# Kernel optimization log

Measured on AMD Instinct MI355X. Metric: run time of the kernel, lower is better.

Reference implementation:

```python
import jax, jax.numpy as jnp
import numpy as np

B, N, C = 4, 4096, 16
HID, OUT = 64, 64
ALL_K, K = 128, 32          # k + k_pos = 32
KD, KDP = 8, 6              # k_dilated, k_dilated_pos
EPS = 1e-5
NEG_SLOPE = 0.2


def setup_inputs() -> dict:
    ks = jax.random.split(jax.random.key(0), 12)
    C2, C4 = 2 * C, 4 * C
    return {
        "x": jax.random.normal(ks[0], (B, N, C), jnp.float32),
        "pos": jax.random.normal(ks[1], (B, N, 3), jnp.float32),
        "W1": jax.random.normal(ks[2], (C2, C2), jnp.float32) * 0.1,
        "g1": jnp.ones((C2,), jnp.float32),
        "b1": jnp.zeros((C2,), jnp.float32),
        "W2": jax.random.normal(ks[3], (HID, C4), jnp.float32) * 0.05,
        "g2": jnp.ones((HID,), jnp.float32),
        "b2": jnp.zeros((HID,), jnp.float32),
        "W3": jax.random.normal(ks[4], (OUT, HID), jnp.float32) * 0.05,
        "g3": jnp.ones((OUT,), jnp.float32),
        "b3": jnp.zeros((OUT,), jnp.float32),
    }


def pdist2(a):
    # squared pairwise distances (same top-k ordering as cdist p=2, and
    # avoids sqrt(0) on the diagonal). a: (B,N,D) -> (B,N,N)
    sq = jnp.sum(a * a, axis=-1)
    d = sq[:, :, None] + sq[:, None, :] - 2.0 * jnp.einsum('bnd,bmd->bnm', a, a)
    return jnp.maximum(d, 0.0)


def knn_excl_self(d2, k):
    # k nearest excluding self (self is the unique 0-distance nearest point)
    idx = jax.lax.top_k(-d2, k + 1)[1]
    return idx[..., 1:]


def fps(pts, npoint):
    # pts: (M, Kn, 3). Deterministic start at index 0 (torch version uses a
    # random start; only the sampled index set differs, math is identical).
    M, Kn, _ = pts.shape
    rows = jnp.arange(M)

    def body(i, state):
        centroids, distance, farthest = state
        centroids = centroids.at[:, i].set(farthest)
        centroid = pts[rows, farthest][:, None, :]            # (M,1,3)
        dist = jnp.sum((pts - centroid) ** 2, axis=-1)         # (M,Kn)
        distance = jnp.minimum(distance, dist)
        farthest = jnp.argmax(distance, axis=-1).astype(jnp.int32)
        return centroids, distance, farthest

    init = (jnp.zeros((M, npoint), jnp.int32),
            jnp.full((M, Kn), 1e10, jnp.float32),
            jnp.zeros((M,), jnp.int32))
    centroids, _, _ = jax.lax.fori_loop(0, npoint, body, init)
    return centroids


def edge_feat(feat, idx):
    # feat: (B,N,D) node features, idx: (B,N,Kn) neighbor indices
    # returns cat(neighbor - center, center): (B,N,Kn,2D)  (edge_function 249)
    nbr = feat[jnp.arange(feat.shape[0])[:, None, None], idx]  # (B,N,Kn,D)
    ctr = feat[:, :, None, :]
    return jnp.concatenate([nbr - ctr, jnp.broadcast_to(ctr, nbr.shape)], axis=-1)


def bn_lrelu(h, g, b):
    # BatchNorm2d with track_running_stats=False -> always batch stats.
    # h: (B,N,Kn,Cc), stats over (B,N,Kn) per channel.
    mu = jnp.mean(h, axis=(0, 1, 2), keepdims=True)
    var = jnp.var(h, axis=(0, 1, 2), keepdims=True)
    h = (h - mu) * jax.lax.rsqrt(var + EPS) * g + b
    return jnp.where(h > 0, h, NEG_SLOPE * h)


def reference(x, pos, W1, g1, b1, W2, g2, b2, W3, g3, b3):
    # --- dilated neighborhood: all_k nearest by position, FPS down to k ---
    cd2 = pdist2(pos)                                   # (B,N,N)
    idx_l = jax.lax.top_k(-cd2, ALL_K)[1]               # (B,N,ALL_K) incl. self
    idx_l_flat = idx_l.reshape(B * N, ALL_K)
    pts = pos.reshape(B * N, 3)[idx_l_flat]             # (B*N, ALL_K, 3)
    idx_fps_local = fps(pts, K)                         # (B*N, K)
    idx_fps = jnp.take_along_axis(idx_l_flat, idx_fps_local, axis=1)
    idx_fps = idx_fps.reshape(B, N, K)                  # (B,N,K)

    # --- dual kNN graph: k_dilated by feature distance + k_dilated_pos by pos ---
    idx_feat = knn_excl_self(pdist2(x), KD)             # (B,N,KD)
    idx_pos = knn_excl_self(cd2, KDP)                   # (B,N,KDP)
    idx1 = jnp.concatenate([idx_feat, idx_pos], axis=2)  # (B,N,KD+KDP)

    # --- conv1x1-BN-LeakyReLU on dual-graph edge features, max over nbrs ---
    e1 = edge_feat(x, idx1)                             # (B,N,14,2C)
    h1 = bn_lrelu(jnp.einsum('bnkc,oc->bnko', e1, W1), g1, b1)
    f1 = jnp.max(h1, axis=2)                            # (B,N,2C)

    # --- edge features on FPS-dilated graph, two conv1x1-BN-LeakyReLU ---
    e2 = edge_feat(f1, idx_fps)                         # (B,N,K,4C)
    h2 = bn_lrelu(jnp.einsum('bnkc,hc->bnkh', e2, W2), g2, b2)
    h3 = bn_lrelu(jnp.einsum('bnkh,oh->bnko', h2, W3), g3, b3)
    out = jnp.max(h3, axis=2)                           # (B,N,OUT)
    return out, idx1
```

## Files before the change

### kernel.cpp

```cpp
#include <hip/hip_runtime.h>

#define NPTS 4096
#define BNROWS 16384

__device__ __forceinline__ float lrelu(float h) { return h > 0.f ? h : 0.2f * h; }

#define WSYNC asm volatile("s_waitcnt lgkmcnt(0)" ::: "memory")

__device__ __forceinline__ float rfl(float v) {
  return __int_as_float(__builtin_amdgcn_readfirstlane(__float_as_int(v)));
}

__global__ __launch_bounds__(256) void norms_kernel(
    const float* __restrict__ x, float* __restrict__ sqx)
{
  int r = blockIdx.x * 256 + threadIdx.x;
  const float4* xp = (const float4*)(x + (size_t)r * 16);
  float4 a0 = xp[0], a1 = xp[1], a2 = xp[2], a3 = xp[3];
  float s = a0.x*a0.x + a0.y*a0.y + a0.z*a0.z + a0.w*a0.w
          + a1.x*a1.x + a1.y*a1.y + a1.z*a1.z + a1.w*a1.w
          + a2.x*a2.x + a2.y*a2.y + a2.z*a2.z + a2.w*a2.w
          + a3.x*a3.x + a3.y*a3.y + a3.z*a3.z + a3.w*a3.w;
  sqx[r] = s;
}

__global__ __launch_bounds__(512) void knn_pos_kernel(
    const float* __restrict__ pos, int* __restrict__ idx_l,
    int* __restrict__ idx1_i, float* __restrict__ idx1_f)
{
  __shared__ unsigned long long cKey[8][512];
  __shared__ unsigned int cCnt[8];
  int tid = threadIdx.x;
  int w = tid >> 6, lane = tid & 63;
  int r = blockIdx.x * 8 + w;
  int b = r >> 12, n = r & 4095;
  const float* pb = pos + (size_t)b * NPTS * 3;
  float cx = pb[n*3+0], cy = pb[n*3+1], cz = pb[n*3+2];
  if (lane == 0) cCnt[w] = 0u;
  WSYNC;

  unsigned int qp[32];
  int m1 = 65536, m2 = 65536, m3 = 65536;
  #pragma unroll
  for (int t = 0; t < 32; ++t) {
    unsigned int wq = 0u;
    #pragma unroll
    for (int h = 0; h < 2; ++h) {
      int j = (2*t + h) * 64 + lane;
      float dx = cx - pb[j*3+0], dy = cy - pb[j*3+1], dz = cz - pb[j*3+2];
      float d2 = dx*dx + dy*dy + dz*dz;
      int q = (int)(d2 * 1000.0f);
      q = q < 0 ? 0 : (q > 65535 ? 65535 : q);
      wq |= ((unsigned int)q) << (16*h);
      int nm1 = min(m1, q);
      int nm2 = min(m2, max(m1, q));
      int nm3 = min(m3, max(m2, q));
      m1 = nm1; m2 = nm2; m3 = nm3;
    }
    qp[t] = wq;
  }
  int lo = 0, hi = 65535;
  #pragma unroll
  for (int it = 0; it < 16; ++it) {
    int mid = (lo + hi) >> 1;
    int cnt = __popcll(__ballot(m3 <= mid));
    if (cnt >= 43) hi = mid; else lo = mid + 1;
  }
  unsigned int qt = (unsigned int)lo + 2u;

  #pragma unroll
  for (int t = 0; t < 32; ++t) {
    unsigned int wq = qp[t];
    unsigned int q0 = wq & 0xffffu, q1 = wq >> 16;
    if (q0 <= qt) { unsigned int p = atomicAdd(&cCnt[w], 1u); if (p < 512u) cKey[w][p] = (unsigned long long)((2*t)*64 + lane); }
    if (q1 <= qt) { unsigned int p = atomicAdd(&cCnt[w], 1u); if (p < 512u) cKey[w][p] = (unsigned long long)((2*t+1)*64 + lane); }
  }
  WSYNC;
  unsigned int nc = cCnt[w]; if (nc > 512u) nc = 512u;
  int M = (nc <= 256u) ? 256 : 512;
  int EPL = M >> 6;

  double cxd = (double)cx, cyd = (double)cy, czd = (double)cz;
  for (int t = 0; t < EPL; ++t) {
    int c = lane + (t << 6);
    unsigned long long kk = ~0ull;
    if (c < (int)nc) {
      int id = (int)cKey[w][c];
      double dx = cxd - (double)pb[id*3+0];
      double dy = cyd - (double)pb[id*3+1];
      double dz = czd - (double)pb[id*3+2];
      double d2 = dx*dx + dy*dy + dz*dz;
      unsigned long long bits = (unsigned long long)__double_as_longlong(d2);
      kk = (bits & ~0xFFFull) | (unsigned long long)(unsigned int)id;
    }
    cKey[w][c] = kk;
  }
  WSYNC;

  for (int k = 2; k <= M; k <<= 1) {
    for (int j = k >> 1; j > 0; j >>= 1) {
      for (int t = 0; t < EPL; ++t) {
        int i = lane + (t << 6);
        int ixj = i ^ j;
        if (ixj > i) {
          unsigned long long ka = cKey[w][i], kb = cKey[w][ixj];
          bool up = ((i & k) == 0);
          if ((ka > kb) == up) { cKey[w][i] = kb; cKey[w][ixj] = ka; }
        }
      }
      WSYNC;
    }
  }
  idx_l[(size_t)r * 128 + lane]      = (int)(cKey[w][lane] & 0xFFFull);
  idx_l[(size_t)r * 128 + lane + 64] = (int)(cKey[w][lane + 64] & 0xFFFull);
  if (lane < 6) {
    int v = (int)(cKey[w][1 + lane] & 0xFFFull);
    idx1_i[r * 14 + 8 + lane] = v;
    idx1_f[r * 14 + 8 + lane] = (float)v;
  }
}

__global__ __launch_bounds__(256) void knn_feat_kernel(
    const float* __restrict__ x, const float* __restrict__ sqx,
    int* __restrict__ idx1_i, float* __restrict__ idx1_f)
{
  __shared__ float lmin[4][256];
  __shared__ int cand[4][192];
  __shared__ unsigned int cCnt[4];
  __shared__ float qtS[4];
  __shared__ float ctrf[4][16];
  int tid = threadIdx.x;
  int w = tid >> 6, lane = tid & 63;
  int rbase = blockIdx.x * 4;
  int b = rbase >> 12;
  const float* xb = x + (size_t)b * NPTS * 16;
  const float* sqb = sqx + b * NPTS;

  if (tid < 64) {
    int rr = tid >> 4, c = tid & 15;
    ctrf[rr][c] = xb[(size_t)((rbase + rr) & 4095) * 16 + c];
  }
  if (tid < 4) cCnt[tid] = 0u;
  __syncthreads();

  float cm[4][16], c2[4];
  #pragma unroll
  for (int rr = 0; rr < 4; ++rr) {
    float s = 0.f;
    #pragma unroll
    for (int c = 0; c < 16; ++c) {
      float v = ctrf[rr][c];
      cm[rr][c] = rfl(-2.0f * v);
      s = fmaf(v, v, s);
    }
    c2[rr] = rfl(s);
  }

  float key[4][16];
  float fk[4] = {3.4e38f, 3.4e38f, 3.4e38f, 3.4e38f};
  #pragma unroll
  for (int pt = 0; pt < 16; ++pt) {
    int j = tid + 256 * pt;
    const float4* xj = (const float4*)(xb + (size_t)j * 16);
    float4 a0 = xj[0], a1 = xj[1], a2 = xj[2], a3 = xj[3];
    float sqj = sqb[j];
    float va[16] = {a0.x,a0.y,a0.z,a0.w, a1.x,a1.y,a1.z,a1.w,
                    a2.x,a2.y,a2.z,a2.w, a3.x,a3.y,a3.z,a3.w};
    #pragma unroll
    for (int rr = 0; rr < 4; ++rr) {
      float acc = sqj + c2[rr];
      #pragma unroll
      for (int c = 0; c < 16; ++c) acc = fmaf(va[c], cm[rr][c], acc);
      key[rr][pt] = acc;
      fk[rr] = fminf(fk[rr], acc);
    }
  }
  #pragma unroll
  for (int rr = 0; rr < 4; ++rr) lmin[rr][tid] = fk[rr];
  __syncthreads();

  {
    float lv0 = lmin[w][lane], lv1 = lmin[w][lane + 64];
    float lv2 = lmin[w][lane + 128], lv3 = lmin[w][lane + 192];
    unsigned int lo = 0u, hi = 0x7F800000u;
    for (int it = 0; it < 31; ++it) {
      unsigned int mid = (lo + hi) >> 1;
      float midf = __uint_as_float(mid);
      int cnt = __popcll(__ballot(lv0 <= midf)) + __popcll(__ballot(lv1 <= midf))
              + __popcll(__ballot(lv2 <= midf)) + __popcll(__ballot(lv3 <= midf));
      if (cnt >= 10) hi = mid; else lo = mid + 1;
    }
    if (lane == 0) qtS[w] = __uint_as_float(hi) * 1.0002f + 1e-3f;
  }
  __syncthreads();

  {
    float q0 = qtS[0], q1 = qtS[1], q2 = qtS[2], q3 = qtS[3];
    #pragma unroll
    for (int pt = 0; pt < 16; ++pt) {
      int j = tid + 256 * pt;
      if (key[0][pt] <= q0) { unsigned int p = atomicAdd(&cCnt[0], 1u); if (p < 192u) cand[0][p] = j; }
      if (key[1][pt] <= q1) { unsigned int p = atomicAdd(&cCnt[1], 1u); if (p < 192u) cand[1][p] = j; }
      if (key[2][pt] <= q2) { unsigned int p = atomicAdd(&cCnt[2], 1u); if (p < 192u) cand[2][p] = j; }
      if (key[3][pt] <= q3) { unsigned int p = atomicAdd(&cCnt[3], 1u); if (p < 192u) cand[3][p] = j; }
    }
  }
  __syncthreads();

  {
    int nc = (int)cCnt[w]; if (nc > 192) nc = 192;
    double key64[3]; int kid[3];
    #pragma unroll
    for (int s = 0; s < 3; ++s) {
      int c = lane + 64*s;
      if (c < nc) {
        int id = cand[w][c];
        const float4* xp = (const float4*)(xb + (size_t)id * 16);
        float4 q0 = xp[0], q1 = xp[1], q2 = xp[2], q3 = xp[3];
        float xv[16] = {q0.x,q0.y,q0.z,q0.w, q1.x,q1.y,q1.z,q1.w,
                        q2.x,q2.y,q2.z,q2.w, q3.x,q3.y,q3.z,q3.w};
        double acc = 0.0;
        #pragma unroll
        for (int c2i = 0; c2i < 16; ++c2i) { double d = (double)ctrf[w][c2i] - (double)xv[c2i]; acc += d * d; }
        key64[s] = acc; kid[s] = id;
      } else { key64[s] = 1e300; kid[s] = 0x7fffffff; }
    }
    int row = rbase + w;
    for (int it = 0; it < 9; ++it) {
      double bk = key64[0]; int bi = kid[0], bs = 0;
      if (key64[1] < bk || (key64[1] == bk && kid[1] < bi)) { bk = key64[1]; bi = kid[1]; bs = 1; }
      if (key64[2] < bk || (key64[2] == bk && kid[2] < bi)) { bk = key64[2]; bi = kid[2]; bs = 2; }
      double rk = bk; int ri = bi;
      #pragma unroll
      for (int off = 32; off > 0; off >>= 1) {
        double ok = __shfl_xor(rk, off, 64);
        int oi = __shfl_xor(ri, off, 64);
        if (ok < rk || (ok == rk && oi < ri)) { rk = ok; ri = oi; }
      }
      if (it > 0 && lane == 0) {
        idx1_i[row * 14 + it - 1] = ri;
        idx1_f[row * 14 + it - 1] = (float)ri;
      }
      if (bi == ri) key64[bs] = 1e300;
    }
  }
}

__global__ __launch_bounds__(256) void fps_kernel(
    const float* __restrict__ pos, const int* __restrict__ idx_l, int* __restrict__ idx_fps)
{
  int wave = threadIdx.x >> 6, lane = threadIdx.x & 63;
  int r = blockIdx.x * 4 + wave;
  const int* il = idx_l + (size_t)r * 128;
  int gi0 = il[lane], gi1 = il[lane + 64];
  double x0 = (double)pos[gi0*3+0], y0 = (double)pos[gi0*3+1], z0 = (double)pos[gi0*3+2];
  double x1 = (double)pos[gi1*3+0], y1 = (double)pos[gi1*3+1], z1 = (double)pos[gi1*3+2];
  double d0 = 1e10, d1 = 1e10;
  int far = 0;
  int* outp = idx_fps + (size_t)r * 32;
  for (int i = 0; i < 32; ++i) {
    int ownerLane = far & 63;
    int sel = far >> 6;
    int gsel = sel ? gi1 : gi0;
    int gout = __shfl(gsel, ownerLane, 64);
    if (lane == 0) outp[i] = gout;
    double cx = __shfl(sel ? x1 : x0, ownerLane, 64);
    double cy = __shfl(sel ? y1 : y0, ownerLane, 64);
    double cz = __shfl(sel ? z1 : z0, ownerLane, 64);
    double t0 = (x0-cx)*(x0-cx) + (y0-cy)*(y0-cy) + (z0-cz)*(z0-cz);
    double t1 = (x1-cx)*(x1-cx) + (y1-cy)*(y1-cy) + (z1-cz)*(z1-cz);
    d0 = fmin(d0, t0); d1 = fmin(d1, t1);
    double v; int p;
    if (d1 > d0) { v = d1; p = lane + 64; } else { v = d0; p = lane; }
    for (int off = 32; off > 0; off >>= 1) {
      double ov = __shfl_xor(v, off, 64);
      int op = __shfl_xor(p, off, 64);
      if (ov > v || (ov == v && op < p)) { v = ov; p = op; }
    }
    far = p;
  }
}

__global__ __launch_bounds__(256) void sv_kernel(
    const float* __restrict__ x, const float* __restrict__ W1,
    float* __restrict__ s, float* __restrict__ v)
{
  __shared__ float xs[8][16];
  __shared__ float w1t[512], w1dt[512];
  int tid = threadIdx.x;
  int rbase = blockIdx.x * 8;
  for (int i = tid; i < 512; i += 256) {
    int c = i >> 5, o = i & 31;
    float a = W1[o * 32 + c], bb = W1[o * 32 + 16 + c];
    w1t[i] = a; w1dt[i] = bb - a;
  }
  if (tid < 128) { int rr = tid >> 4, c = tid & 15; xs[rr][c] = x[(size_t)(rbase + rr) * 16 + c]; }
  __syncthreads();
  int rr = tid >> 5, o = tid & 31;
  float sa = 0.f, va = 0.f;
  #pragma unroll
  for (int c = 0; c < 16; ++c) {
    float xv = xs[rr][c];
    sa = fmaf(xv, w1t[c * 32 + o], sa);
    va = fmaf(xv, w1dt[c * 32 + o], va);
  }
  int r = rbase + rr;
  s[(size_t)r * 32 + o] = sa;
  v[(size_t)r * 32 + o] = va;
}

__global__ __launch_bounds__(256) void h1stats_kernel(
    const float* __restrict__ s, const float* __restrict__ v, const int* __restrict__ idx1_i,
    double* __restrict__ slotsH1, float* __restrict__ h1max)
{
  __shared__ int sidx[8][14];
  __shared__ float sred[256], sred2[256];
  int tid = threadIdx.x;
  int rr = tid >> 5, o = tid & 31;
  int rbase = blockIdx.x * 8;
  if (tid < 112) { int q = tid / 14, k = tid % 14; sidx[q][k] = idx1_i[(rbase + q) * 14 + k]; }
  __syncthreads();
  int r = rbase + rr;
  int broff = r & ~4095;
  float vv = v[(size_t)r * 32 + o];
  float m = -3.4e38f, ls = 0.f, lss = 0.f;
  #pragma unroll
  for (int k = 0; k < 14; ++k) {
    int j = sidx[rr][k];
    float val = s[(size_t)(broff + j) * 32 + o] + vv;
    m = fmaxf(m, val);
    ls += val; lss += val * val;
  }
  h1max[(size_t)r * 32 + o] = m;
  sred[tid] = ls; sred2[tid] = lss;
  __syncthreads();
  if (tid < 32) {
    float s2 = 0.f, ss = 0.f;
    #pragma unroll
    for (int j = 0; j < 8; ++j) { s2 += sred[j * 32 + tid]; ss += sred2[j * 32 + tid]; }
    int slot = blockIdx.x & 255;
    atomicAdd(&slotsH1[slot * 64 + tid], (double)s2);
    atomicAdd(&slotsH1[slot * 64 + 32 + tid], (double)ss);
  }
}

__global__ void finalize_stats_kernel(const double* __restrict__ slots, int C, double cnt,
    const float* __restrict__ g, const float* __restrict__ bta, float* __restrict__ scsh)
{
  int o = threadIdx.x;
  if (o < C) {
    double s = 0.0, ss = 0.0;
    for (int slot = 0; slot < 256; ++slot) { s += slots[slot * 2 * C + o]; ss += slots[slot * 2 * C + C + o]; }
    double mu = s / cnt;
    double var = ss / cnt - mu * mu;
    double rs = 1.0 / sqrt(var + 1e-5);
    float sc = (float)rs * g[o];
    float sh = bta[o] - (float)mu * sc;
    scsh[o] = sc;
    scsh[C + o] = sh;
  }
}

__global__ __launch_bounds__(256) void tu_kernel(
    const float* __restrict__ h1max, const float* __restrict__ scsh1, const float* __restrict__ W2,
    float* __restrict__ t, float* __restrict__ u)
{
  __shared__ float f1s[4][32];
  __shared__ float w2t[2048], w2dt[2048];
  int tid = threadIdx.x;
  int rbase = blockIdx.x * 4;
  for (int i = tid; i < 2048; i += 256) {
    int c = i >> 6, o = i & 63;
    float a = W2[o * 64 + c], bb = W2[o * 64 + 32 + c];
    w2t[i] = a; w2dt[i] = bb - a;
  }
  if (tid < 128) {
    int rr = tid >> 5, c = tid & 31;
    f1s[rr][c] = lrelu(h1max[(size_t)(rbase + rr) * 32 + c] * scsh1[c] + scsh1[32 + c]);
  }
  __syncthreads();
  int rr = tid >> 6, o = tid & 63;
  float ta = 0.f, ua = 0.f;
  #pragma unroll
  for (int c = 0; c < 32; ++c) {
    float fv = f1s[rr][c];
    ta = fmaf(fv, w2t[c * 64 + o], ta);
    ua = fmaf(fv, w2dt[c * 64 + o], ua);
  }
  int r = rbase + rr;
  t[(size_t)r * 64 + o] = ta;
  u[(size_t)r * 64 + o] = ua;
}

__global__ __launch_bounds__(256) void h2stats_kernel(
    const float* __restrict__ t, const float* __restrict__ u, const int* __restrict__ idx_fps,
    double* __restrict__ slotsH2)
{
  __shared__ int nids[8][32];
  __shared__ float sred[256], sred2[256];
  int tid = threadIdx.x;
  int o = tid & 63, wv = tid >> 6;
  int rbase = blockIdx.x * 8;
  { int q = tid >> 5, k = tid & 31; nids[q][k] = idx_fps[(rbase + q) * 32 + k]; }
  __syncthreads();
  float ls = 0.f, lss = 0.f;
  for (int rr = 0; rr < 8; ++rr) {
    int r = rbase + rr;
    int broff = r & ~4095;
    float uo = u[(size_t)r * 64 + o];
    #pragma unroll
    for (int i = 0; i < 8; ++i) {
      int k = wv + 4 * i;
      float val = t[(size_t)(broff + nids[rr][k]) * 64 + o] + uo;
      ls += val; lss += val * val;
    }
  }
  sred[tid] = ls; sred2[tid] = lss;
  __syncthreads();
  if (tid < 64) {
    float s2 = sred[tid] + sred[tid + 64] + sred[tid + 128] + sred[tid + 192];
    float ss = sred2[tid] + sred2[tid + 64] + sred2[tid + 128] + sred2[tid + 192];
    int slot = blockIdx.x & 255;
    atomicAdd(&slotsH2[slot * 128 + tid], (double)s2);
    atomicAdd(&slotsH2[slot * 128 + 64 + tid], (double)ss);
  }
}

#define ROWS3 8
__global__ __launch_bounds__(256, 4) void h3_kernel(
    const float* __restrict__ t, const float* __restrict__ u, const int* __restrict__ idx_fps,
    const float* __restrict__ W3, const float* __restrict__ scsh2,
    double* __restrict__ slotsH3, float* __restrict__ h3max)
{
  __shared__ float h2lds[2048];
  __shared__ float wmax[256];
  __shared__ float sred[256], sred2[256];
  __shared__ int nids[ROWS3][32];
  int tid = threadIdx.x;
  int o = tid & 63, wv = tid >> 6;
  float4 w3r[16];
  const float4* w3p = (const float4*)(W3 + o * 64);
  #pragma unroll
  for (int j = 0; j < 16; ++j) w3r[j] = w3p[j];
  float sc2o = scsh2[o], sh2o = scsh2[64 + o];
  int rbase = blockIdx.x * ROWS3;
  { int q = tid >> 5, k = tid & 31; nids[q][k] = idx_fps[(rbase + q) * 32 + k]; }
  float ls = 0.f, lss = 0.f;
  __syncthreads();
  for (int rr = 0; rr < ROWS3; ++rr) {
    int r = rbase + rr;
    int broff = r & ~4095;
    float uo = u[(size_t)r * 64 + o];
    #pragma unroll
    for (int i = 0; i < 8; ++i) {
      int k = wv + 4 * i;
      float val = t[(size_t)(broff + nids[rr][k]) * 64 + o] + uo;
      h2lds[k * 64 + o] = lrelu(val * sc2o + sh2o);
    }
    __syncthreads();
    float kmax = -3.4e38f;
    #pragma unroll
    for (int i = 0; i < 8; ++i) {
      int k = wv + 4 * i;
      const float4* hp = (const float4*)(h2lds + k * 64);
      float acc = 0.f;
      #pragma unroll
      for (int j = 0; j < 16; ++j) {
        float4 h = hp[j];
        acc = fmaf(h.x, w3r[j].x, acc); acc = fmaf(h.y, w3r[j].y, acc);
        acc = fmaf(h.z, w3r[j].z, acc); acc = fmaf(h.w, w3r[j].w, acc);
      }
      ls += acc; lss += acc * acc;
      kmax = fmaxf(kmax, acc);
    }
    wmax[tid] = kmax;
    __syncthreads();
    if (tid < 64) {
      float m = fmaxf(fmaxf(wmax[tid], wmax[64 + tid]), fmaxf(wmax[128 + tid], wmax[192 + tid]));
      h3max[(size_t)r * 64 + tid] = m;
    }
  }
  sred[tid] = ls; sred2[tid] = lss;
  __syncthreads();
  if (tid < 64) {
    float s2 = sred[tid] + sred[tid + 64] + sred[tid + 128] + sred[tid + 192];
    float ss = sred2[tid] + sred2[tid + 64] + sred2[tid + 128] + sred2[tid + 192];
    int slot = blockIdx.x & 255;
    atomicAdd(&slotsH3[slot * 128 + tid], (double)s2);
    atomicAdd(&slotsH3[slot * 128 + 64 + tid], (double)ss);
  }
}

__global__ void out_kernel(const float* __restrict__ h3max, const float* __restrict__ scsh3,
                           float* __restrict__ out)
{
  int i = blockIdx.x * 256 + threadIdx.x;
  int o = i & 63;
  out[i] = lrelu(h3max[i] * scsh3[o] + scsh3[64 + o]);
}

extern "C" void kernel_launch(void* const* d_in, const int* in_sizes, int n_in,
                              void* d_out, int out_size, void* d_ws, size_t ws_size,
                              hipStream_t stream) {
  (void)in_sizes; (void)n_in; (void)out_size; (void)ws_size;
  const float* x   = (const float*)d_in[0];
  const float* pos = (const float*)d_in[1];
  const float* W1  = (const float*)d_in[2];
  const float* g1  = (const float*)d_in[3];
  const float* b1  = (const float*)d_in[4];
  const float* W2  = (const float*)d_in[5];
  const float* g2  = (const float*)d_in[6];
  const float* b2  = (const float*)d_in[7];
  const float* W3  = (const float*)d_in[8];
  const float* g3  = (const float*)d_in[9];
  const float* b3  = (const float*)d_in[10];

  float* out      = (float*)d_out;
  float* out_idx1 = out + 1048576;

  char* ws = (char*)d_ws;
  double* slotsH1 = (double*)(ws + 0);
  double* slotsH2 = (double*)(ws + 131072);
  double* slotsH3 = (double*)(ws + 393216);
  float*  scsh1   = (float*)(ws + 655360);
  float*  scsh2   = (float*)(ws + 655616);
  float*  scsh3   = (float*)(ws + 656128);
  float*  sqx     = (float*)(ws + 786432);
  int*    idx_l   = (int*)(ws + 1048576);
  float*  t_buf   = (float*)(ws + 1048576);
  float*  u_buf   = (float*)(ws + 5242880);
  int*    idx_fps = (int*)(ws + 9437184);
  int*    idx1_i  = (int*)(ws + 11534336);
  float*  h1max   = (float*)(ws + 12451840);
  float*  s_buf   = (float*)(ws + 14548992);
  float*  v_buf   = (float*)(ws + 16646144);
  float*  h3max   = (float*)(ws + 18743296);

  hipMemsetAsync(d_ws, 0, 656640, stream);

  norms_kernel   <<<dim3(64),   dim3(256), 0, stream>>>(x, sqx);
  knn_pos_kernel <<<dim3(2048), dim3(512), 0, stream>>>(pos, idx_l, idx1_i, out_idx1);
  knn_feat_kernel<<<dim3(4096), dim3(256), 0, stream>>>(x, sqx, idx1_i, out_idx1);
  fps_kernel     <<<dim3(4096), dim3(256), 0, stream>>>(pos, idx_l, idx_fps);
  sv_kernel      <<<dim3(2048), dim3(256), 0, stream>>>(x, W1, s_buf, v_buf);
  h1stats_kernel <<<dim3(2048), dim3(256), 0, stream>>>(s_buf, v_buf, idx1_i, slotsH1, h1max);
  finalize_stats_kernel<<<dim3(1), dim3(64), 0, stream>>>(slotsH1, 32, 229376.0, g1, b1, scsh1);
  tu_kernel      <<<dim3(4096), dim3(256), 0, stream>>>(h1max, scsh1, W2, t_buf, u_buf);
  h2stats_kernel <<<dim3(2048), dim3(256), 0, stream>>>(t_buf, u_buf, idx_fps, slotsH2);
  finalize_stats_kernel<<<dim3(1), dim3(64), 0, stream>>>(slotsH2, 64, 524288.0, g2, b2, scsh2);
  h3_kernel      <<<dim3(2048), dim3(256), 0, stream>>>(t_buf, u_buf, idx_fps, W3, scsh2, slotsH3, h3max);
  finalize_stats_kernel<<<dim3(1), dim3(64), 0, stream>>>(slotsH3, 64, 524288.0, g3, b3, scsh3);
  out_kernel     <<<dim3(4096), dim3(256), 0, stream>>>(h3max, scsh3, out);
}
```

Before: 667.9 us.

## Transpose x and pos to channel-major layout for coalesced kNN distance loads

```diff
diff --git a/kernel.cpp b/kernel.cpp
--- a/kernel.cpp
+++ b/kernel.cpp
@@ -11,22 +11,58 @@
   return __int_as_float(__builtin_amdgcn_readfirstlane(__float_as_int(v)));
 }
 
-__global__ __launch_bounds__(256) void norms_kernel(
-    const float* __restrict__ x, float* __restrict__ sqx)
-{
-  int r = blockIdx.x * 256 + threadIdx.x;
-  const float4* xp = (const float4*)(x + (size_t)r * 16);
-  float4 a0 = xp[0], a1 = xp[1], a2 = xp[2], a3 = xp[3];
-  float s = a0.x*a0.x + a0.y*a0.y + a0.z*a0.z + a0.w*a0.w
-          + a1.x*a1.x + a1.y*a1.y + a1.z*a1.z + a1.w*a1.w
-          + a2.x*a2.x + a2.y*a2.y + a2.z*a2.z + a2.w*a2.w
-          + a3.x*a3.x + a3.y*a3.y + a3.z*a3.z + a3.w*a3.w;
-  sqx[r] = s;
+__global__ __launch_bounds__(256) void xpose_kernel(
+    const float* __restrict__ x, float* __restrict__ xT, float* __restrict__ sqx)
+{
+  __shared__ float tile[64][17];
+  int t = threadIdx.x;
+  int j0 = blockIdx.x * 64;
+  int b = j0 >> 12;
+  int jloc0 = j0 & 4095;
+  int p = t >> 2, q = t & 3;
+  const float4* xp = (const float4*)(x + (size_t)(j0 + p) * 16);
+  float4 v = xp[q];
+  tile[p][q*4+0] = v.x; tile[p][q*4+1] = v.y; tile[p][q*4+2] = v.z; tile[p][q*4+3] = v.w;
+  __syncthreads();
+  int jj = t & 63, chi = t >> 6;
+  float* xTb = xT + (size_t)b * 65536;
+  #pragma unroll
+  for (int i = 0; i < 4; ++i) {
+    int c = chi * 4 + i;
+    xTb[c * 4096 + jloc0 + jj] = tile[jj][c];
+  }
+  if (t < 64) {
+    float s = 0.f;
+    #pragma unroll
+    for (int c = 0; c < 16; ++c) { float vv = tile[t][c]; s = fmaf(vv, vv, s); }
+    sqx[j0 + t] = s;
+  }
+}
+
+__global__ __launch_bounds__(192) void ppose_kernel(
+    const float* __restrict__ pos, float* __restrict__ posT)
+{
+  __shared__ float raw[768];
+  int t = threadIdx.x;
+  int j0 = blockIdx.x * 256;
+  int b = j0 >> 12;
+  int jloc0 = j0 & 4095;
+  const float4* pp = (const float4*)(pos + (size_t)j0 * 3);
+  float4 v = pp[t];
+  raw[t*4+0] = v.x; raw[t*4+1] = v.y; raw[t*4+2] = v.z; raw[t*4+3] = v.w;
+  __syncthreads();
+  float* pTb = posT + (size_t)b * 12288;
+  #pragma unroll
+  for (int i = 0; i < 4; ++i) {
+    int idx = t + 192 * i;
+    int c = idx >> 8, jj = idx & 255;
+    pTb[c * 4096 + jloc0 + jj] = raw[jj * 3 + c];
+  }
 }
 
 __global__ __launch_bounds__(512) void knn_pos_kernel(
-    const float* __restrict__ pos, int* __restrict__ idx_l,
-    int* __restrict__ idx1_i, float* __restrict__ idx1_f)
+    const float* __restrict__ pos, const float* __restrict__ posT,
+    int* __restrict__ idx_l, int* __restrict__ idx1_i, float* __restrict__ idx1_f)
 {
   __shared__ unsigned long long cKey[8][512];
   __shared__ unsigned int cCnt[8];
@@ -35,6 +71,7 @@
   int r = blockIdx.x * 8 + w;
   int b = r >> 12, n = r & 4095;
   const float* pb = pos + (size_t)b * NPTS * 3;
+  const float* pT = posT + (size_t)b * 12288;
   float cx = pb[n*3+0], cy = pb[n*3+1], cz = pb[n*3+2];
   if (lane == 0) cCnt[w] = 0u;
   WSYNC;
@@ -47,7 +84,7 @@
     #pragma unroll
     for (int h = 0; h < 2; ++h) {
       int j = (2*t + h) * 64 + lane;
-      float dx = cx - pb[j*3+0], dy = cy - pb[j*3+1], dz = cz - pb[j*3+2];
+      float dx = cx - pT[j], dy = cy - pT[4096 + j], dz = cz - pT[8192 + j];
       float d2 = dx*dx + dy*dy + dz*dz;
       int q = (int)(d2 * 1000.0f);
       q = q < 0 ? 0 : (q > 65535 ? 65535 : q);
@@ -121,7 +158,8 @@
 }
 
 __global__ __launch_bounds__(256) void knn_feat_kernel(
-    const float* __restrict__ x, const float* __restrict__ sqx,
+    const float* __restrict__ x, const float* __restrict__ xT,
+    const float* __restrict__ sqx,
     int* __restrict__ idx1_i, float* __restrict__ idx1_f)
 {
   __shared__ float lmin[4][256];
@@ -133,7 +171,8 @@
   int w = tid >> 6, lane = tid & 63;
   int rbase = blockIdx.x * 4;
   int b = rbase >> 12;
-  const float* xb = x + (size_t)b * NPTS * 16;
+  const float* xb  = x  + (size_t)b * NPTS * 16;
+  const float* xTb = xT + (size_t)b * 65536;
   const float* sqb = sqx + b * NPTS;
 
   if (tid < 64) {
@@ -161,19 +200,19 @@
   #pragma unroll
   for (int pt = 0; pt < 16; ++pt) {
     int j = tid + 256 * pt;
-    const float4* xj = (const float4*)(xb + (size_t)j * 16);
-    float4 a0 = xj[0], a1 = xj[1], a2 = xj[2], a3 = xj[3];
     float sqj = sqb[j];
-    float va[16] = {a0.x,a0.y,a0.z,a0.w, a1.x,a1.y,a1.z,a1.w,
-                    a2.x,a2.y,a2.z,a2.w, a3.x,a3.y,a3.z,a3.w};
-    #pragma unroll
-    for (int rr = 0; rr < 4; ++rr) {
-      float acc = sqj + c2[rr];
-      #pragma unroll
-      for (int c = 0; c < 16; ++c) acc = fmaf(va[c], cm[rr][c], acc);
-      key[rr][pt] = acc;
-      fk[rr] = fminf(fk[rr], acc);
-    }
+    float a0 = sqj + c2[0], a1 = sqj + c2[1], a2 = sqj + c2[2], a3 = sqj + c2[3];
+    #pragma unroll
+    for (int c = 0; c < 16; ++c) {
+      float va = xTb[c * 4096 + j];
+      a0 = fmaf(va, cm[0][c], a0);
+      a1 = fmaf(va, cm[1][c], a1);
+      a2 = fmaf(va, cm[2][c], a2);
+      a3 = fmaf(va, cm[3][c], a3);
+    }
+    key[0][pt] = a0; key[1][pt] = a1; key[2][pt] = a2; key[3][pt] = a3;
+    fk[0] = fminf(fk[0], a0); fk[1] = fminf(fk[1], a1);
+    fk[2] = fminf(fk[2], a2); fk[3] = fminf(fk[3], a3);
   }
   #pragma unroll
   for (int rr = 0; rr < 4; ++rr) lmin[rr][tid] = fk[rr];
@@ -517,6 +556,7 @@
 
   float* out      = (float*)d_out;
   float* out_idx1 = out + 1048576;
+  float* xT       = out;
 
   char* ws = (char*)d_ws;
   double* slotsH1 = (double*)(ws + 0);
@@ -526,6 +566,7 @@
   float*  scsh2   = (float*)(ws + 655616);
   float*  scsh3   = (float*)(ws + 656128);
   float*  sqx     = (float*)(ws + 786432);
+  float*  posT    = (float*)(ws + 851968);
   int*    idx_l   = (int*)(ws + 1048576);
   float*  t_buf   = (float*)(ws + 1048576);
   float*  u_buf   = (float*)(ws + 5242880);
@@ -538,9 +579,10 @@
 
   hipMemsetAsync(d_ws, 0, 656640, stream);
 
-  norms_kernel   <<<dim3(64),   dim3(256), 0, stream>>>(x, sqx);
-  knn_pos_kernel <<<dim3(2048), dim3(512), 0, stream>>>(pos, idx_l, idx1_i, out_idx1);
-  knn_feat_kernel<<<dim3(4096), dim3(256), 0, stream>>>(x, sqx, idx1_i, out_idx1);
+  xpose_kernel   <<<dim3(256),  dim3(256), 0, stream>>>(x, xT, sqx);
+  ppose_kernel   <<<dim3(64),   dim3(192), 0, stream>>>(pos, posT);
+  knn_pos_kernel <<<dim3(2048), dim3(512), 0, stream>>>(pos, posT, idx_l, idx1_i, out_idx1);
+  knn_feat_kernel<<<dim3(4096), dim3(256), 0, stream>>>(x, xT, sqx, idx1_i, out_idx1);
   fps_kernel     <<<dim3(4096), dim3(256), 0, stream>>>(pos, idx_l, idx_fps);
   sv_kernel      <<<dim3(2048), dim3(256), 0, stream>>>(x, W1, s_buf, v_buf);
   h1stats_kernel <<<dim3(2048), dim3(256), 0, stream>>>(s_buf, v_buf, idx1_i, slotsH1, h1max);
```

Result: slower. 732.8 us (+9.7%).

## Move positional kNN bitonic sort from LDS into registers with wave shuffles

Applied to the files above, without the earlier changes.

```diff
diff --git a/kernel.cpp b/kernel.cpp
--- a/kernel.cpp
+++ b/kernel.cpp
@@ -9,6 +9,12 @@
 
 __device__ __forceinline__ float rfl(float v) {
   return __int_as_float(__builtin_amdgcn_readfirstlane(__float_as_int(v)));
+}
+
+__device__ __forceinline__ unsigned long long shflx64(unsigned long long v, int m) {
+  int lo = __shfl_xor((int)(unsigned int)(v & 0xffffffffull), m, 64);
+  int hi = __shfl_xor((int)(unsigned int)(v >> 32), m, 64);
+  return ((unsigned long long)(unsigned int)hi << 32) | (unsigned int)lo;
 }
 
 __global__ __launch_bounds__(256) void norms_kernel(
@@ -28,7 +34,7 @@
     const float* __restrict__ pos, int* __restrict__ idx_l,
     int* __restrict__ idx1_i, float* __restrict__ idx1_f)
 {
-  __shared__ unsigned long long cKey[8][512];
+  __shared__ int cand[8][512];
   __shared__ unsigned int cCnt[8];
   int tid = threadIdx.x;
   int w = tid >> 6, lane = tid & 63;
@@ -72,20 +78,20 @@
   for (int t = 0; t < 32; ++t) {
     unsigned int wq = qp[t];
     unsigned int q0 = wq & 0xffffu, q1 = wq >> 16;
-    if (q0 <= qt) { unsigned int p = atomicAdd(&cCnt[w], 1u); if (p < 512u) cKey[w][p] = (unsigned long long)((2*t)*64 + lane); }
-    if (q1 <= qt) { unsigned int p = atomicAdd(&cCnt[w], 1u); if (p < 512u) cKey[w][p] = (unsigned long long)((2*t+1)*64 + lane); }
+    if (q0 <= qt) { unsigned int p = atomicAdd(&cCnt[w], 1u); if (p < 512u) cand[w][p] = (2*t)*64 + lane; }
+    if (q1 <= qt) { unsigned int p = atomicAdd(&cCnt[w], 1u); if (p < 512u) cand[w][p] = (2*t+1)*64 + lane; }
   }
   WSYNC;
   unsigned int nc = cCnt[w]; if (nc > 512u) nc = 512u;
-  int M = (nc <= 256u) ? 256 : 512;
-  int EPL = M >> 6;
 
   double cxd = (double)cx, cyd = (double)cy, czd = (double)cz;
-  for (int t = 0; t < EPL; ++t) {
-    int c = lane + (t << 6);
+  unsigned long long key[8];
+  #pragma unroll
+  for (int t = 0; t < 8; ++t) {
+    int c = (t << 6) | lane;
     unsigned long long kk = ~0ull;
     if (c < (int)nc) {
-      int id = (int)cKey[w][c];
+      int id = cand[w][c];
       double dx = cxd - (double)pb[id*3+0];
       double dy = cyd - (double)pb[id*3+1];
       double dz = czd - (double)pb[id*3+2];
@@ -93,30 +99,46 @@
       unsigned long long bits = (unsigned long long)__double_as_longlong(d2);
       kk = (bits & ~0xFFFull) | (unsigned long long)(unsigned int)id;
     }
-    cKey[w][c] = kk;
-  }
-  WSYNC;
-
-  for (int k = 2; k <= M; k <<= 1) {
-    for (int j = k >> 1; j > 0; j >>= 1) {
-      for (int t = 0; t < EPL; ++t) {
-        int i = lane + (t << 6);
-        int ixj = i ^ j;
-        if (ixj > i) {
-          unsigned long long ka = cKey[w][i], kb = cKey[w][ixj];
-          bool up = ((i & k) == 0);
-          if ((ka > kb) == up) { cKey[w][i] = kb; cKey[w][ixj] = ka; }
+    key[t] = kk;
+  }
+
+  #pragma unroll
+  for (int kk2 = 1; kk2 <= 9; ++kk2) {
+    const int k = 1 << kk2;
+    #pragma unroll
+    for (int jj = kk2 - 1; jj >= 0; --jj) {
+      const int j = 1 << jj;
+      if (j >= 64) {
+        const int jt = j >> 6;
+        #pragma unroll
+        for (int t = 0; t < 8; ++t) {
+          const int tp = t ^ jt;
+          if (tp > t) {
+            const bool up = (((t << 6) & k) == 0);
+            unsigned long long a = key[t], bq = key[tp];
+            if ((a > bq) == up) { key[t] = bq; key[tp] = a; }
+          }
+        }
+      } else {
+        #pragma unroll
+        for (int t = 0; t < 8; ++t) {
+          unsigned long long p = shflx64(key[t], j);
+          bool up = ((((t << 6) | lane) & k) == 0);
+          bool lower = ((lane & j) == 0);
+          unsigned long long mn = (key[t] < p) ? key[t] : p;
+          unsigned long long mx = (key[t] < p) ? p : key[t];
+          key[t] = (lower == up) ? mn : mx;
         }
       }
-      WSYNC;
-    }
-  }
-  idx_l[(size_t)r * 128 + lane]      = (int)(cKey[w][lane] & 0xFFFull);
-  idx_l[(size_t)r * 128 + lane + 64] = (int)(cKey[w][lane + 64] & 0xFFFull);
-  if (lane < 6) {
-    int v = (int)(cKey[w][1 + lane] & 0xFFFull);
-    idx1_i[r * 14 + 8 + lane] = v;
-    idx1_f[r * 14 + 8 + lane] = (float)v;
+    }
+  }
+
+  idx_l[(size_t)r * 128 + lane]      = (int)(key[0] & 0xFFFull);
+  idx_l[(size_t)r * 128 + lane + 64] = (int)(key[1] & 0xFFFull);
+  if (lane >= 1 && lane < 7) {
+    int v = (int)(key[0] & 0xFFFull);
+    idx1_i[r * 14 + 8 + (lane - 1)] = v;
+    idx1_f[r * 14 + 8 + (lane - 1)] = (float)v;
   }
 }
 
```

Measured after the change: 666.1 us. About the same (-0.3%).
